# Kernel tuning notes

Hardware: AMD Instinct MI355X
Metric: run time of the kernel (lower is better)

The kernel has to match this reference:

```python
import jax, jax.numpy as jnp
import numpy as np

B, T, D = 4, 4000, 1024
H = 8
DK = D // H          # key dim per head; value dim per head also DK (value_factor=1)
CHUNK = 500
EPS_LN = 1e-5
EPS_RMS = 1e-6


def rotate_every_two(x):
    x1 = x[..., ::2]
    x2 = x[..., 1::2]
    return jnp.stack((-x2, x1), axis=-1).reshape(x.shape)


def theta_shift(x, sin, cos):
    # x: [b,h,t,dk]; sin/cos: [t,dk]
    return x * cos + rotate_every_two(x) * sin


def rel_pos(slen, chunk_len, num_heads, key_dim):
    # RetNetRelPos(chunkwise_recurrent=True)
    angle = 1.0 / (10000 ** jnp.linspace(0.0, 1.0, key_dim // 2))
    angle = jnp.repeat(angle, 2)  # == unsqueeze(-1).repeat(1,2).flatten()
    decay = jnp.log(1.0 - 2.0 ** (-5.0 - jnp.arange(num_heads, dtype=jnp.float32)))
    index = jnp.arange(slen, dtype=jnp.float32)
    sin = jnp.sin(index[:, None] * angle[None, :])  # [t,dk]
    cos = jnp.cos(index[:, None] * angle[None, :])
    bi = jnp.arange(chunk_len, dtype=jnp.float32)
    tril = jnp.tril(jnp.ones((chunk_len, chunk_len), bool))
    diff = bi[:, None] - bi[None, :]
    mask = jnp.where(tril[None], jnp.exp(decay[:, None, None] * diff[None]), 0.0)  # [H,C,C]
    last_row = mask[:, -1]                                            # [H,C]
    value_inner_decay = (last_row / last_row.sum(-1, keepdims=True))[:, :, None]  # [H,C,1]
    scale = jnp.sqrt(mask.sum(-1, keepdims=True))                     # [H,C,1]
    inner_mask = mask / scale
    cross_decay = jnp.exp(decay * chunk_len)[:, None, None]           # [H,1,1]
    qid = jnp.exp(decay[:, None] * (bi + 1.0))[:, :, None]            # [H,C,1]
    query_inner_decay = qid / (scale / last_row.sum(-1)[:, None, None])
    return (sin, cos), (inner_mask, cross_decay, query_inner_decay, value_inner_decay)


def retention_chunkwise(qr, kr, v, inner):
    mask, cross_decay, query_inner_decay, value_inner_decay = inner
    b, t = v.shape[0], v.shape[1]
    C = mask.shape[1]
    n = t // C
    h, dk = qr.shape[1], qr.shape[3]
    dv = v.shape[2] // h
    # [b,h,t,dk] -> [b,n,h,C,dk]
    qr = qr.transpose(0, 2, 1, 3).reshape(b, n, C, h, dk).transpose(0, 1, 3, 2, 4)
    kr = kr.transpose(0, 2, 1, 3).reshape(b, n, C, h, dk).transpose(0, 1, 3, 2, 4)
    v = v.reshape(b, n, C, h, dv).transpose(0, 1, 3, 2, 4)  # [b,n,h,C,dv]

    qk = jnp.einsum('bnhcd,bnhed->bnhce', qr, kr) * mask  # [b,n,h,C,C]
    inner_scale = jnp.clip(jnp.abs(jax.lax.stop_gradient(qk)).sum(-1, keepdims=True), 1.0, None)
    qk = qk / inner_scale
    inner_output = jnp.einsum('bnhce,bnhed->bnhcd', qk, v)  # [b,n,h,C,dv]

    kv = jnp.einsum('bnhck,bnhcv->bnhkv', kr, v * value_inner_decay)  # [b,n,h,dk,dv]

    def step(carry, kv_i):
        kv_state, kv_scale = carry
        out = (kv_state / kv_scale, kv_scale)
        new_state = kv_state * cross_decay + kv_i
        sg = jnp.abs(jax.lax.stop_gradient(new_state)).sum(-2, keepdims=True).max(-1, keepdims=True)
        return (new_state, jnp.clip(sg, 1.0, None)), out

    init = (jnp.zeros((b, h, dk, dv), v.dtype), jnp.ones((b, h, 1, 1), v.dtype))
    _, (kv_rec, cross_scale) = jax.lax.scan(step, init, jnp.moveaxis(kv, 1, 0))
    kv_rec = jnp.moveaxis(kv_rec, 0, 1)            # [b,n,h,dk,dv]
    cross_scale = jnp.moveaxis(cross_scale, 0, 1)  # [b,n,h,1,1]

    all_scale = jnp.maximum(inner_scale, cross_scale)
    cross_output = jnp.einsum('bnhcd,bnhdv->bnhcv', qr * query_inner_decay, kv_rec)
    output = inner_output / (all_scale / inner_scale) + cross_output / (all_scale / cross_scale)
    return output.transpose(0, 1, 3, 2, 4).reshape(b, t, h, dv)  # [b,t,h,dv]


def setup_inputs() -> dict:
    key = jax.random.key(0)
    ks = jax.random.split(key, 6)
    s = 0.02
    return {
        'inputs': jax.random.normal(ks[0], (B, T, D), jnp.float32),
        'ln_gamma': jnp.ones((D,), jnp.float32),
        'ln_beta': jnp.zeros((D,), jnp.float32),
        'Wq': jax.random.normal(ks[1], (D, D), jnp.float32) * s,
        'Wk': jax.random.normal(ks[2], (D, D), jnp.float32) * s,
        'Wv': jax.random.normal(ks[3], (D, D), jnp.float32) * s,
        'Wg': jax.random.normal(ks[4], (D, D), jnp.float32) * s,
        'Wo': jax.random.normal(ks[5], (D, D), jnp.float32) * s,
    }


def reference(inputs, ln_gamma, ln_beta, Wq, Wk, Wv, Wg, Wo):
    b, t, d = inputs.shape
    # pre-LayerNorm
    mu = inputs.mean(-1, keepdims=True)
    var = ((inputs - mu) ** 2).mean(-1, keepdims=True)
    x = (inputs - mu) / jnp.sqrt(var + EPS_LN) * ln_gamma + ln_beta

    (sin, cos), inner = rel_pos(t, CHUNK, H, DK)

    q = (x @ Wq).reshape(b, t, H, DK).transpose(0, 2, 1, 3)
    k = (x @ Wk * (DK ** -0.5)).reshape(b, t, H, DK).transpose(0, 2, 1, 3)
    v = x @ Wv
    g = x @ Wg

    qr = theta_shift(q, sin, cos)
    kr = theta_shift(k, sin, cos)

    out = retention_chunkwise(qr, kr, v, inner)  # [b,t,H,dv]
    # group norm: per-head RMSNorm without affine
    out = out * jax.lax.rsqrt(jnp.mean(out ** 2, -1, keepdims=True) + EPS_RMS)
    out = out.reshape(b, t, H * DK)
    out = jax.nn.silu(g) * out
    return out @ Wo  # dropout is identity in eval
```

## Files before the change

### kernel.cpp

```cpp
#include <hip/hip_runtime.h>
#include <hip/hip_bf16.h>


typedef __attribute__((ext_vector_type(4))) float f32x4;
typedef __attribute__((ext_vector_type(8))) short s16x8;

#define DEV static __device__ __forceinline__

DEV float bfu(ushort u){ union{uint i; float f;} x; x.i=((uint)u)<<16; return x.f; }
DEV ushort f2bf(float f){ union{float f; uint u;} x; x.f=f; uint r = x.u + 0x7fffu + ((x.u>>16)&1u); return (ushort)(r>>16); }
DEV uint pack2(float lo, float hi){ return ((uint)f2bf(hi)<<16) | (uint)f2bf(lo); }

DEV void gload16(const ushort* g, ushort* l) {
  __builtin_amdgcn_global_load_lds((const __attribute__((address_space(1))) void*)g,
                                   (__attribute__((address_space(3))) void*)l, 16, 0, 0);
}

__global__ __launch_bounds__(256) void f2bf_t_all(const float* __restrict__ s0, const float* __restrict__ s1,
                                                  const float* __restrict__ s2, const float* __restrict__ s3,
                                                  const float* __restrict__ s4,
                                                  ushort* __restrict__ d0, ushort* __restrict__ d1,
                                                  ushort* __restrict__ d2, ushort* __restrict__ d3,
                                                  ushort* __restrict__ d4) {
  const float* src; ushort* dst;
  switch (blockIdx.z) {
    case 0: src=s0; dst=d0; break;
    case 1: src=s1; dst=d1; break;
    case 2: src=s2; dst=d2; break;
    case 3: src=s3; dst=d3; break;
    default: src=s4; dst=d4; break;
  }
  __shared__ ushort t[64][72];
  int kt = blockIdx.x*64, nt = blockIdx.y*64;
  int tid = threadIdx.x;
  int r = tid>>2, c0 = (tid&3)*16;
  const float* s = src + (size_t)(kt+r)*1024 + nt + c0;
  #pragma unroll
  for (int j=0;j<16;j+=4) {
    float4 vv = *(const float4*)(s+j);
    t[r][c0+j]=f2bf(vv.x); t[r][c0+j+1]=f2bf(vv.y); t[r][c0+j+2]=f2bf(vv.z); t[r][c0+j+3]=f2bf(vv.w);
  }
  __syncthreads();
  union { uint4 u4[2]; ushort s16[16]; } tmp;
  #pragma unroll
  for (int j=0;j<16;j++) tmp.s16[j] = t[c0+j][r];
  ushort* d = dst + (size_t)(nt+r)*1024 + kt + c0;
  *(uint4*)(d)   = tmp.u4[0];
  *(uint4*)(d+8) = tmp.u4[1];
}

__global__ __launch_bounds__(256) void ln_kernel(const float* __restrict__ x,
                                                 const float* __restrict__ gamma,
                                                 const float* __restrict__ beta,
                                                 ushort* __restrict__ xo) {
  int row = blockIdx.x;
  int tid = threadIdx.x;
  const float* xr = x + (size_t)row*1024;
  float4 u = ((const float4*)xr)[tid];
  float s = u.x+u.y+u.z+u.w;
  float sq = u.x*u.x+u.y*u.y+u.z*u.z+u.w*u.w;
  #pragma unroll
  for (int o=32;o;o>>=1){ s += __shfl_xor(s,o); sq += __shfl_xor(sq,o); }
  __shared__ float red[8];
  int wv=tid>>6, ln=tid&63;
  if (ln==0){ red[wv]=s; red[4+wv]=sq; }
  __syncthreads();
  s = red[0]+red[1]+red[2]+red[3];
  sq = red[4]+red[5]+red[6]+red[7];
  float mu = s*(1.0f/1024.0f);
  float var = sq*(1.0f/1024.0f)-mu*mu;
  float inv = rsqrtf(var+1e-5f);
  float4 gg = ((const float4*)gamma)[tid];
  float4 bb = ((const float4*)beta)[tid];
  float o0=(u.x-mu)*inv*gg.x+bb.x;
  float o1=(u.y-mu)*inv*gg.y+bb.y;
  float o2=(u.z-mu)*inv*gg.z+bb.z;
  float o3=(u.w-mu)*inv*gg.w+bb.w;
  uint2 w; w.x=pack2(o0,o1); w.y=pack2(o2,o3);
  ((uint2*)(xo+(size_t)row*1024))[tid]=w;
}

__global__ __launch_bounds__(256) void sincos_kernel(float* __restrict__ sint, float* __restrict__ cost) {
  int idx = blockIdx.x*256+threadIdx.x;
  if (idx >= 4000*64) return;
  int t = idx>>6, i = idx&63;
  float ang = expf(-9.210340371976184f * (float)i * (1.0f/63.0f));
  float a = (float)t * ang;
  float sv = sinf(a), cv = cosf(a);
  sint[(size_t)t*128+2*i] = sv; sint[(size_t)t*128+2*i+1] = sv;
  cost[(size_t)t*128+2*i] = cv; cost[(size_t)t*128+2*i+1] = cv;
}

template<int EPI>
__global__ __launch_bounds__(256) void gemm_bt(const ushort* __restrict__ A,
                                               const ushort* __restrict__ BT,
                                               void* __restrict__ Cv,
                                               ushort* __restrict__ kTout,
                                               const float* __restrict__ sint,
                                               const float* __restrict__ cost,
                                               int M, int N, int K) {
  __shared__ ushort As[8192];
  __shared__ ushort Bs[8192];
  int ny = N>>7;
  int cpx = ((M>>7)*ny)>>3;
  int wg = blockIdx.x;
  int orig = (wg&7)*cpx + (wg>>3);
  int bm = (orig>>3)*128, bn = (orig&7)*128;
  int tid = threadIdx.x;
  int w = tid>>6, l = tid&63;
  int wm = (w>>1)*64, wn = (w&1)*64;
  int rsel = l&15, ko = (l>>4)*8;
  f32x4 acc[4][4];
  #pragma unroll
  for (int i=0;i<4;i++)
    #pragma unroll
    for (int j=0;j<4;j++){ acc[i][j][0]=0; acc[i][j][1]=0; acc[i][j][2]=0; acc[i][j][3]=0; }
  const ushort* ap0 = A  + (size_t)(bm + w*32 + (l>>2))*K + (l&3)*8;
  const ushort* ap1 = ap0 + (size_t)16*K;
  const ushort* bp0 = BT + (size_t)(bn + w*32 + (l>>2))*K + (l&3)*8;
  const ushort* bp1 = bp0 + (size_t)16*K;
  {
    ushort* ab = As + w*1024; ushort* bb = Bs + w*1024;
    gload16(ap0, ab); gload16(ap1, ab+512);
    gload16(bp0, bb); gload16(bp1, bb+512);
  }
  int cur = 0;
  for (int kt=0; kt<K; kt+=32) {
    __syncthreads();
    if (kt+32 < K) {
      int nb = cur^1;
      ushort* ab = As + nb*4096 + w*1024; ushort* bb = Bs + nb*4096 + w*1024;
      gload16(ap0+kt+32, ab); gload16(ap1+kt+32, ab+512);
      gload16(bp0+kt+32, bb); gload16(bp1+kt+32, bb+512);
    }
    const ushort* Ac = As + cur*4096;
    const ushort* Bc = Bs + cur*4096;
    s16x8 af[4], bfr[4];
    #pragma unroll
    for (int mf=0;mf<4;mf++) af[mf]  = *(const s16x8*)&Ac[(wm+mf*16+rsel)*32 + ko];
    #pragma unroll
    for (int nf=0;nf<4;nf++) bfr[nf] = *(const s16x8*)&Bc[(wn+nf*16+rsel)*32 + ko];
    #pragma unroll
    for (int mf=0;mf<4;mf++)
      #pragma unroll
      for (int nf=0;nf<4;nf++)
        acc[mf][nf] = __builtin_amdgcn_mfma_f32_16x16x32_bf16(af[mf], bfr[nf], acc[mf][nf], 0,0,0);
    cur ^= 1;
  }
  int crow0 = bm+wm+(l>>4)*4;
  int ccol0 = bn+wn+(l&15);
  #pragma unroll
  for (int mf=0;mf<4;mf++) {
    #pragma unroll
    for (int nf=0;nf<4;nf++) {
      int col = ccol0 + nf*16;
      if constexpr (EPI==0) {
        ushort* C = (ushort*)Cv;
        #pragma unroll
        for (int r2=0;r2<4;r2++)
          C[(size_t)(crow0+mf*16+r2)*N + col] = f2bf(acc[mf][nf][r2]);
      } else if constexpr (EPI==1) {
        float* C = (float*)Cv;
        #pragma unroll
        for (int r2=0;r2<4;r2++)
          C[(size_t)(crow0+mf*16+r2)*N + col] = acc[mf][nf][r2];
      } else if constexpr (EPI==2 || EPI==3) {
        ushort* C = (ushort*)Cv;
        int h = col>>7, d = col&127;
        float decay = logf(1.0f - exp2f(-5.0f-(float)h));
        #pragma unroll
        for (int r2=0;r2<4;r2++) {
          int row = crow0+mf*16+r2;
          int t = row - (row/4000)*4000;
          float cc = cost[(size_t)t*128+d], ss = sint[(size_t)t*128+d];
          float vv = acc[mf][nf][r2];
          float ov = __shfl_xor(vv, 1);
          float rot = ((l&1)==0) ? (vv*cc - ov*ss) : (vv*cc + ov*ss);
          int cch = t - (t/500)*500;
          if constexpr (EPI==2) {
            rot *= expf(decay*(float)cch);
            C[(size_t)row*N + col] = f2bf(rot);
          } else {
            rot *= expf(-decay*(float)cch) * 0.08838834764831845f;
            ushort rb = f2bf(rot);
            C[(size_t)row*N + col] = rb;
            int bnh = (row/4000)*64 + (t/500)*8 + h;
            kTout[(size_t)bnh*65536 + (size_t)d*512 + cch] = rb;
          }
        }
      } else {
        ushort* vTo = (ushort*)Cv;
        int h = col>>7, d = col&127;
        #pragma unroll
        for (int r2=0;r2<4;r2++) {
          int row = crow0+mf*16+r2;
          int t = row - (row/4000)*4000;
          int bnh = (row/4000)*64 + (t/500)*8 + h;
          int cch = t - (t/500)*500;
          vTo[(size_t)bnh*65536 + (size_t)d*512 + cch] = f2bf(acc[mf][nf][r2]);
        }
      }
    }
  }
}

__global__ __launch_bounds__(256) void kv_mfma(const ushort* __restrict__ kT,
                                               const ushort* __restrict__ vT,
                                               float* __restrict__ kvp) {
  int bnh = blockIdx.x;
  __shared__ ushort sh2[16384];
  int tid=threadIdx.x;
  int wv=tid>>6, l=tid&63, g=l>>4, c16=l&15;
  int wr = wv>>1, wc = wv&1;
  int ri[4], ro[4];
  #pragma unroll
  for (int jj=0;jj<4;jj++){
    int i = wv*256 + jj*64 + l;
    ri[jj] = i>>3;
    ro[jj] = (((i&7)*16) ^ ((ri[jj]&7)<<4))>>1;
  }
  const ushort* kbase = kT + (size_t)bnh*65536;
  const ushort* vbase = vT + (size_t)bnh*65536;
  f32x4 acc[4][4];
  #pragma unroll
  for (int i=0;i<4;i++)
    #pragma unroll
    for (int j=0;j<4;j++){ acc[i][j][0]=0; acc[i][j][1]=0; acc[i][j][2]=0; acc[i][j][3]=0; }
  for (int ctep=0; ctep<8; ctep++) {
    int cb = ctep*64;
    __syncthreads();
    #pragma unroll
    for (int jj=0;jj<4;jj++){
      gload16(kbase + (size_t)ri[jj]*512 + cb + ro[jj], (ushort*)((char*)sh2 + wv*4096 + jj*1024));
      gload16(vbase + (size_t)ri[jj]*512 + cb + ro[jj], (ushort*)((char*)sh2 + 16384 + wv*4096 + jj*1024));
    }
    __syncthreads();
    if (ctep==7) {
      for (int z=tid; z<128*12; z+=256) {
        int r = z/12, j = 52 + (z - (z/12)*12);
        *(ushort*)((char*)sh2 + 16384 + r*128 + ((j*2) ^ ((r&7)<<4))) = 0;
      }
      __syncthreads();
    }
    #pragma unroll
    for (int kc=0;kc<2;kc++) {
      s16x8 af[4], bf2[4];
      #pragma unroll
      for (int mf=0;mf<4;mf++){
        int row = wr*64+mf*16+c16;
        af[mf] = *(const s16x8*)((const char*)sh2 + row*128 + ((((kc*32+g*8)*2)) ^ ((row&7)<<4)));
      }
      #pragma unroll
      for (int nf=0;nf<4;nf++){
        int row = wc*64+nf*16+c16;
        bf2[nf] = *(const s16x8*)((const char*)sh2 + 16384 + row*128 + ((((kc*32+g*8)*2)) ^ ((row&7)<<4)));
      }
      #pragma unroll
      for (int mf=0;mf<4;mf++)
        #pragma unroll
        for (int nf=0;nf<4;nf++)
          acc[mf][nf] = __builtin_amdgcn_mfma_f32_16x16x32_bf16(af[mf], bf2[nf], acc[mf][nf], 0,0,0);
    }
  }
  float* outp = kvp + (size_t)bnh*16384;
  #pragma unroll
  for (int mf=0;mf<4;mf++)
    #pragma unroll
    for (int nf=0;nf<4;nf++)
      #pragma unroll
      for (int reg=0;reg<4;reg++)
        outp[(size_t)(wr*64+mf*16+g*4+reg)*128 + wc*64+nf*16+c16] = acc[mf][nf][reg];
}

__global__ __launch_bounds__(256) void scan_kernel(const float* __restrict__ kvp,
                                                   ushort* __restrict__ kvrecT,
                                                   float* __restrict__ crosssc) {
  int bh = blockIdx.x;
  int b = bh>>3, h = bh&7;
  float Dh = 1.0f - exp2f(-5.0f-(float)h);
  float decay = logf(Dh);
  float cd = expf(decay*500.0f);
  float ls = (1.0f - expf(decay*500.0f))/(1.0f-Dh);
  float cst = expf(decay*499.0f)/ls;
  int tid=threadIdx.x;
  int vcol = tid&127, khalf = tid>>7;
  float st[64];
  #pragma unroll
  for (int i=0;i<64;i++) st[i]=0;
  float scale = 1.0f;
  __shared__ float colpart[2][128];
  __shared__ float sred[2];
  for (int n=0;n<8;n++) {
    int bnh = (b*8+n)*8+h;
    const float* src = kvp + (size_t)bnh*16384;
    ushort* rec = kvrecT + (size_t)bnh*16384;
    float inv = 1.0f/scale;
    float cs = 0;
    #pragma unroll
    for (int i=0;i<64;i++) {
      int kk = khalf*64+i;
      rec[(size_t)vcol*128+kk] = f2bf(st[i]*inv);
      st[i] = st[i]*cd + cst*src[(size_t)kk*128+vcol];
      cs += fabsf(st[i]);
    }
    if (tid==0) crosssc[bnh] = scale;
    colpart[khalf][vcol] = cs;
    __syncthreads();
    if (tid<128) colpart[0][tid] += colpart[1][tid];
    __syncthreads();
    float m = (tid<128)? colpart[0][tid] : 0.0f;
    #pragma unroll
    for (int o=32;o;o>>=1) m = fmaxf(m,__shfl_xor(m,o));
    if (tid<128 && (tid&63)==0) sred[tid>>6]=m;
    __syncthreads();
    scale = fmaxf(fmaxf(sred[0],sred[1]),1.0f);
    __syncthreads();
  }
}

__global__ __launch_bounds__(256,4) void iout_mfma(const ushort* __restrict__ qr,
                                                   const ushort* __restrict__ kr,
                                                   const ushort* __restrict__ vT,
                                                   const ushort* __restrict__ kvrecT,
                                                   const float* __restrict__ crosssc,
                                                   const ushort* __restrict__ gbuf,
                                                   ushort* __restrict__ opre) {
  int ib = blockIdx.x;
  int x = ib&7, u = ib>>3;
  int rt = u&7;
  int bnh = x*32 + (u>>3);
  int h = bnh&7, n=(bnh>>3)&7, b=bnh>>6;
  size_t base = (size_t)(b*4000+n*500)*1024 + h*128;
  float Dh = 1.0f - exp2f(-5.0f-(float)h);
  float decay = logf(Dh);
  __shared__ ushort sh[20480];
  char* shb = (char*)sh;
  int tid = threadIdx.x;
  int wv = tid>>6, l = tid&63;
  int g = l>>4, c16 = l&15;
  int r_base = rt*64 + wv*16 + g*4;

  int qrow = rt*64 + wv*16 + c16; if (qrow>499) qrow=499;
  s16x8 aq[4];
  #pragma unroll
  for (int kc=0;kc<4;kc++)
    aq[kc] = *(const s16x8*)(qr + base + (size_t)qrow*1024 + kc*32 + g*8);

  int ktrow[4], ktofs[4], vtrow[4], vtofs[4];
  #pragma unroll
  for (int jj=0;jj<4;jj++){
    int i = wv*256 + jj*64 + l;
    int r_ = i>>4;  ktrow[jj]=r_;  ktofs[jj] = (((i&15)*16) ^ ((r_&7)<<4))>>1;
    int r2_ = i>>3; vtrow[jj]=r2_; vtofs[jj] = (((i&7)*16) ^ ((r2_&7)<<4))>>1;
  }
  const ushort* vTb = vT + (size_t)bnh*65536;

  f32x4 pv[8], cc[8];
  #pragma unroll
  for (int i=0;i<8;i++){
    #pragma unroll
    for (int j=0;j<4;j++){ pv[i][j]=0.0f; cc[i][j]=0.0f; }
  }
  float rowsum[4] = {0,0,0,0};

  for (int et=0; et<=rt; et++) {
    __syncthreads();
    #pragma unroll
    for (int jj=0;jj<4;jj++){
      int gr = et*64 + ktrow[jj]; if (gr>499) gr=499;
      gload16(kr + base + (size_t)gr*1024 + ktofs[jj], (ushort*)(shb + wv*4096 + jj*1024));
      gload16(vTb + (size_t)vtrow[jj]*512 + et*64 + vtofs[jj], (ushort*)(shb + 16384 + wv*4096 + jj*1024));
    }
    __syncthreads();
    f32x4 S[4];
    #pragma unroll
    for (int i=0;i<4;i++){ S[i][0]=0; S[i][1]=0; S[i][2]=0; S[i][3]=0; }
    __builtin_amdgcn_s_setprio(1);
    #pragma unroll
    for (int kc=0;kc<4;kc++) {
      #pragma unroll
      for (int ni=0;ni<4;ni++) {
        int krow = ni*16+c16;
        s16x8 bf = *(const s16x8*)(shb + krow*256 + ((((kc*32+g*8)*2)) ^ ((krow&7)<<4)));
        S[ni] = __builtin_amdgcn_mfma_f32_16x16x32_bf16(aq[kc], bf, S[ni], 0,0,0);
      }
    }
    __builtin_amdgcn_s_setprio(0);
    bool diag = (et==rt);
    #pragma unroll
    for (int ni=0;ni<4;ni++) {
      int e_rel = et*64 + ni*16 + c16;
      #pragma unroll
      for (int reg=0;reg<4;reg++) {
        float p = S[ni][reg];
        if (diag && e_rel > r_base+reg) p = 0.0f;
        rowsum[reg] += fabsf(p);
        int prow = wv*16 + g*4 + reg;
        *(ushort*)(shb + 32768 + prow*128 + (((ni*16+c16)*2) ^ ((prow&7)<<4))) = f2bf(p);
      }
    }
    __builtin_amdgcn_s_setprio(1);
    #pragma unroll
    for (int kc=0;kc<2;kc++) {
      int prow = wv*16 + c16;
      s16x8 pa = *(const s16x8*)(shb + 32768 + prow*128 + ((((kc*32+g*8)*2)) ^ ((prow&7)<<4)));
      #pragma unroll
      for (int nf=0;nf<8;nf++) {
        int vrow = nf*16+c16;
        s16x8 vb = *(const s16x8*)(shb + 16384 + vrow*128 + ((((kc*32+g*8)*2)) ^ ((vrow&7)<<4)));
        pv[nf] = __builtin_amdgcn_mfma_f32_16x16x32_bf16(pa, vb, pv[nf], 0,0,0);
      }
    }
    __builtin_amdgcn_s_setprio(0);
  }
  #pragma unroll
  for (int reg=0;reg<4;reg++) {
    float s = rowsum[reg];
    s += __shfl_xor(s,1); s += __shfl_xor(s,2); s += __shfl_xor(s,4); s += __shfl_xor(s,8);
    rowsum[reg] = s;
  }
  __syncthreads();
  #pragma unroll
  for (int jj=0;jj<8;jj++){
    int i = wv*512 + jj*64 + l;
    int r_ = i>>4;
    int ofs = (((i&15)*16) ^ ((r_&7)<<4))>>1;
    gload16(kvrecT + (size_t)bnh*16384 + (size_t)r_*128 + ofs, (ushort*)(shb + wv*8192 + jj*1024));
  }
  __syncthreads();
  __builtin_amdgcn_s_setprio(1);
  #pragma unroll
  for (int kc=0;kc<4;kc++) {
    #pragma unroll
    for (int nf=0;nf<8;nf++) {
      int krow = nf*16+c16;
      s16x8 bb = *(const s16x8*)(shb + krow*256 + ((((kc*32+g*8)*2)) ^ ((krow&7)<<4)));
      cc[nf] = __builtin_amdgcn_mfma_f32_16x16x32_bf16(aq[kc], bb, cc[nf], 0,0,0);
    }
  }
  __builtin_amdgcn_s_setprio(0);
  float cs = crosssc[bnh];
  float lsum = (1.0f-expf(decay*500.0f))/(1.0f-Dh);
  float ed = expf(decay);
  #pragma unroll
  for (int reg=0;reg<4;reg++) {
    int rr = r_base + reg;
    if (rr < 500) {
      float rs = (1.0f-expf(decay*(float)(rr+1)))/(1.0f-Dh);
      float rsr = rsqrtf(rs);
      float is = fmaxf(1.0f, rowsum[reg]*rsr);
      float all = fmaxf(is, cs);
      float qid = ed*lsum*rsr;
      float fi = rsr/all;
      float fc = qid*(cs/all);
      float o[8]; float ssq = 0.0f;
      #pragma unroll
      for (int nf=0;nf<8;nf++){ o[nf] = pv[nf][reg]*fi + cc[nf][reg]*fc; ssq += o[nf]*o[nf]; }
      ssq += __shfl_xor(ssq,1); ssq += __shfl_xor(ssq,2); ssq += __shfl_xor(ssq,4); ssq += __shfl_xor(ssq,8);
      float rmss = rsqrtf(ssq*(1.0f/128.0f)+1e-6f);
      size_t rowoff = (size_t)(b*4000+n*500+rr)*1024 + h*128;
      #pragma unroll
      for (int nf=0;nf<8;nf++){
        float gv = bfu(gbuf[rowoff + nf*16 + c16]);
        float sg = gv/(1.0f+expf(-gv));
        opre[rowoff + nf*16 + c16] = f2bf(sg*o[nf]*rmss);
      }
    }
  }
}

extern "C" void kernel_launch(void* const* d_in, const int* in_sizes, int n_in,
                              void* d_out, int out_size, void* d_ws, size_t ws_size,
                              hipStream_t stream) {
  const float* x     = (const float*)d_in[0];
  const float* gamma = (const float*)d_in[1];
  const float* beta  = (const float*)d_in[2];
  const float* Wq    = (const float*)d_in[3];
  const float* Wk    = (const float*)d_in[4];
  const float* Wv    = (const float*)d_in[5];
  const float* Wg    = (const float*)d_in[6];
  const float* Wo    = (const float*)d_in[7];
  float* out = (float*)d_out;

  char* ws = (char*)d_ws;
  size_t off = 0;
  auto alloc = [&](size_t bytes)->void* { void* p = ws+off; off += (bytes+255)&~(size_t)255; return p; };
  const size_t BT1024 = (size_t)16000*1024;
  ushort* xln  = (ushort*)alloc(BT1024*2);
  ushort* q    = (ushort*)alloc(BT1024*2);
  ushort* k    = (ushort*)alloc(BT1024*2);
  ushort* g    = (ushort*)alloc(BT1024*2);
  ushort* WqT  = (ushort*)alloc((size_t)1024*1024*2);
  ushort* WkT  = (ushort*)alloc((size_t)1024*1024*2);
  ushort* WvT  = (ushort*)alloc((size_t)1024*1024*2);
  ushort* WgT  = (ushort*)alloc((size_t)1024*1024*2);
  ushort* WoT  = (ushort*)alloc((size_t)1024*1024*2);
  float* sint  = (float*)alloc((size_t)4000*128*4);
  float* cost  = (float*)alloc((size_t)4000*128*4);
  ushort* kT   = (ushort*)alloc((size_t)256*65536*2);
  ushort* vT   = (ushort*)alloc((size_t)256*65536*2);
  ushort* kvrecT=(ushort*)alloc((size_t)256*16384*2);
  float* crosssc = (float*)alloc(256*4);
  (void)ws_size; (void)in_sizes; (void)n_in; (void)out_size;

  ln_kernel<<<16000,256,0,stream>>>(x,gamma,beta,xln);
  sincos_kernel<<<1000,256,0,stream>>>(sint,cost);
  dim3 tt(16,16,5);
  f2bf_t_all<<<tt,256,0,stream>>>(Wq,Wk,Wv,Wg,Wo, WqT,WkT,WvT,WgT,WoT);

  gemm_bt<2><<<1000,256,0,stream>>>(xln,WqT,(void*)q, nullptr,sint,cost,16000,1024,1024);
  gemm_bt<3><<<1000,256,0,stream>>>(xln,WkT,(void*)k, kT,     sint,cost,16000,1024,1024);
  gemm_bt<4><<<1000,256,0,stream>>>(xln,WvT,(void*)vT,nullptr,sint,cost,16000,1024,1024);
  gemm_bt<0><<<1000,256,0,stream>>>(xln,WgT,(void*)g, nullptr,sint,cost,16000,1024,1024);

  float* kvp = (float*)xln;
  kv_mfma<<<256,256,0,stream>>>(kT,vT,kvp);
  scan_kernel<<<32,256,0,stream>>>(kvp,kvrecT,crosssc);

  ushort* opre = xln;
  iout_mfma<<<2048,256,0,stream>>>(q,k,vT,kvrecT,crosssc,g,opre);

  gemm_bt<1><<<1000,256,0,stream>>>(opre,WoT,(void*)out,nullptr,sint,cost,16000,1024,1024);
}
```

Baseline: 453.2 us.

## Fuse Q/K/V/G projections into one GEMM with LDS-staged coalesced epilogues

Replaces the four separate projection GEMM launches with one launch that treats the four transposed weight matrices as a single N=4096 operand. Each tile's output is staged through shared memory so q/k/g rows are written with 16-byte vector stores and the transposed kT/vT chunk layouts are written as packed 8-element vectors. Previously these were scattered 2-byte stores. The output GEMM also stages fp32 results through LDS for coalesced float4 writes. The fused kernel assumes WqT, WkT, WvT and WgT sit contiguously in the workspace, and it adds extra LDS use and barriers in the epilogue.

```diff
diff --git a/kernel.cpp b/kernel.cpp
--- a/kernel.cpp
+++ b/kernel.cpp
@@ -91,20 +91,145 @@
   cost[(size_t)t*128+2*i] = cv; cost[(size_t)t*128+2*i+1] = cv;
 }
 
-template<int EPI>
-__global__ __launch_bounds__(256) void gemm_bt(const ushort* __restrict__ A,
-                                               const ushort* __restrict__ BT,
-                                               void* __restrict__ Cv,
-                                               ushort* __restrict__ kTout,
-                                               const float* __restrict__ sint,
-                                               const float* __restrict__ cost,
-                                               int M, int N, int K) {
-  __shared__ ushort As[8192];
-  __shared__ ushort Bs[8192];
-  int ny = N>>7;
-  int cpx = ((M>>7)*ny)>>3;
+__global__ __launch_bounds__(256) void gemm_proj(const ushort* __restrict__ A,
+                                                 const ushort* __restrict__ BT,
+                                                 ushort* __restrict__ qb,
+                                                 ushort* __restrict__ kb,
+                                                 ushort* __restrict__ gb,
+                                                 ushort* __restrict__ kT,
+                                                 ushort* __restrict__ vT,
+                                                 const float* __restrict__ sint,
+                                                 const float* __restrict__ cost) {
+  __attribute__((aligned(16))) __shared__ char smem[34816];
+  ushort* As = (ushort*)smem;
+  ushort* Bs = (ushort*)(smem+16384);
+  const int K = 1024;
   int wg = blockIdx.x;
-  int orig = (wg&7)*cpx + (wg>>3);
+  int orig = (wg&7)*500 + (wg>>3);
+  int bm = (orig>>5)*128, bn = (orig&31)*128;
+  int tid = threadIdx.x;
+  int w = tid>>6, l = tid&63;
+  int wm = (w>>1)*64, wn = (w&1)*64;
+  int rsel = l&15, ko = (l>>4)*8;
+  f32x4 acc[4][4];
+  #pragma unroll
+  for (int i=0;i<4;i++)
+    #pragma unroll
+    for (int j=0;j<4;j++){ acc[i][j][0]=0; acc[i][j][1]=0; acc[i][j][2]=0; acc[i][j][3]=0; }
+  const ushort* ap0 = A  + (size_t)(bm + w*32 + (l>>2))*K + (l&3)*8;
+  const ushort* ap1 = ap0 + (size_t)16*K;
+  const ushort* bp0 = BT + (size_t)(bn + w*32 + (l>>2))*K + (l&3)*8;
+  const ushort* bp1 = bp0 + (size_t)16*K;
+  {
+    ushort* ab = As + w*1024; ushort* bb2 = Bs + w*1024;
+    gload16(ap0, ab); gload16(ap1, ab+512);
+    gload16(bp0, bb2); gload16(bp1, bb2+512);
+  }
+  int cur = 0;
+  for (int kt=0; kt<K; kt+=32) {
+    __syncthreads();
+    if (kt+32 < K) {
+      int nb = cur^1;
+      ushort* ab = As + nb*4096 + w*1024; ushort* bb2 = Bs + nb*4096 + w*1024;
+      gload16(ap0+kt+32, ab); gload16(ap1+kt+32, ab+512);
+      gload16(bp0+kt+32, bb2); gload16(bp1+kt+32, bb2+512);
+    }
+    const ushort* Ac = As + cur*4096;
+    const ushort* Bc = Bs + cur*4096;
+    s16x8 af[4], bfr[4];
+    #pragma unroll
+    for (int mf=0;mf<4;mf++) af[mf]  = *(const s16x8*)&Ac[(wm+mf*16+rsel)*32 + ko];
+    #pragma unroll
+    for (int nf=0;nf<4;nf++) bfr[nf] = *(const s16x8*)&Bc[(wn+nf*16+rsel)*32 + ko];
+    #pragma unroll
+    for (int mf=0;mf<4;mf++)
+      #pragma unroll
+      for (int nf=0;nf<4;nf++)
+        acc[mf][nf] = __builtin_amdgcn_mfma_f32_16x16x32_bf16(af[mf], bfr[nf], acc[mf][nf], 0,0,0);
+    cur ^= 1;
+  }
+  int proj = bn>>10;
+  int bnp  = bn&1023;
+  int hh   = bnp>>7;
+  __syncthreads();
+  ushort* Ct = (ushort*)smem;
+  if (proj < 2) {
+    float decay = logf(1.0f - exp2f(-5.0f-(float)hh));
+    float ksc = 0.08838834764831845f;
+    #pragma unroll
+    for (int mf=0;mf<4;mf++) {
+      #pragma unroll
+      for (int r2=0;r2<4;r2++) {
+        int rowt = wm+mf*16+(l>>4)*4+r2;
+        int grow = bm+rowt;
+        int t = grow - (grow/4000)*4000;
+        int cch = t - (t/500)*500;
+        float esc = (proj==0)? expf(decay*(float)cch) : expf(-decay*(float)cch)*ksc;
+        const float* ctab = cost + (size_t)t*128;
+        const float* stab = sint + (size_t)t*128;
+        #pragma unroll
+        for (int nf=0;nf<4;nf++) {
+          int colt = wn+nf*16+(l&15);
+          float vv = acc[mf][nf][r2];
+          float cc = ctab[colt], ss = stab[colt];
+          float ov = __shfl_xor(vv,1);
+          float rot = ((l&1)==0)? (vv*cc-ov*ss) : (vv*cc+ov*ss);
+          Ct[rowt*136+colt] = f2bf(rot*esc);
+        }
+      }
+    }
+  } else {
+    #pragma unroll
+    for (int mf=0;mf<4;mf++)
+      #pragma unroll
+      for (int nf=0;nf<4;nf++) {
+        int colt = wn+nf*16+(l&15);
+        #pragma unroll
+        for (int r2=0;r2<4;r2++)
+          Ct[(wm+mf*16+(l>>4)*4+r2)*136+colt] = f2bf(acc[mf][nf][r2]);
+      }
+  }
+  __syncthreads();
+  if (proj != 2) {
+    ushort* dst = (proj==0)? qb : (proj==1)? kb : gb;
+    int r = tid>>1, ch=(tid&1)*64;
+    ushort* drow = dst + (size_t)(bm+r)*1024 + bnp + ch;
+    #pragma unroll
+    for (int j=0;j<8;j++) *(uint4*)(drow+j*8) = *(uint4*)&Ct[r*136+ch+j*8];
+  }
+  if (proj==1 || proj==2) {
+    ushort* Tdst = (proj==1)? kT : vT;
+    int dloc = tid>>1, rh=(tid&1)*64;
+    #pragma unroll
+    for (int j=0;j<8;j++) {
+      int gr = bm + rh + j*8;
+      int bb = gr/4000; int t0 = gr - bb*4000;
+      int ch0 = t0/500; int c0 = t0 - ch0*500;
+      if (c0 <= 492) {
+        union{uint4 u; ushort s[8];} pk;
+        #pragma unroll
+        for (int i=0;i<8;i++) pk.s[i] = Ct[(rh+j*8+i)*136 + dloc];
+        *(uint4*)(Tdst + ((size_t)(bb*64+ch0*8+hh))*65536 + (size_t)dloc*512 + c0) = pk.u;
+      } else {
+        #pragma unroll
+        for (int i=0;i<8;i++) {
+          int gri = gr+i; int bbi=gri/4000; int ti=gri-bbi*4000; int chi=ti/500; int ci=ti-chi*500;
+          Tdst[((size_t)(bbi*64+chi*8+hh))*65536 + (size_t)dloc*512 + ci] = Ct[(rh+j*8+i)*136+dloc];
+        }
+      }
+    }
+  }
+}
+
+__global__ __launch_bounds__(256) void gemm_out(const ushort* __restrict__ A,
+                                                const ushort* __restrict__ BT,
+                                                float* __restrict__ C) {
+  __attribute__((aligned(16))) __shared__ char smem[34816];
+  ushort* As = (ushort*)smem;
+  ushort* Bs = (ushort*)(smem+16384);
+  const int K = 1024;
+  int wg = blockIdx.x;
+  int orig = (wg&7)*125 + (wg>>3);
   int bm = (orig>>3)*128, bn = (orig&7)*128;
   int tid = threadIdx.x;
   int w = tid>>6, l = tid&63;
@@ -120,18 +245,18 @@
   const ushort* bp0 = BT + (size_t)(bn + w*32 + (l>>2))*K + (l&3)*8;
   const ushort* bp1 = bp0 + (size_t)16*K;
   {
-    ushort* ab = As + w*1024; ushort* bb = Bs + w*1024;
+    ushort* ab = As + w*1024; ushort* bb2 = Bs + w*1024;
     gload16(ap0, ab); gload16(ap1, ab+512);
-    gload16(bp0, bb); gload16(bp1, bb+512);
+    gload16(bp0, bb2); gload16(bp1, bb2+512);
   }
   int cur = 0;
   for (int kt=0; kt<K; kt+=32) {
     __syncthreads();
     if (kt+32 < K) {
       int nb = cur^1;
-      ushort* ab = As + nb*4096 + w*1024; ushort* bb = Bs + nb*4096 + w*1024;
+      ushort* ab = As + nb*4096 + w*1024; ushort* bb2 = Bs + nb*4096 + w*1024;
       gload16(ap0+kt+32, ab); gload16(ap1+kt+32, ab+512);
-      gload16(bp0+kt+32, bb); gload16(bp1+kt+32, bb+512);
+      gload16(bp0+kt+32, bb2); gload16(bp1+kt+32, bb2+512);
     }
     const ushort* Ac = As + cur*4096;
     const ushort* Bc = Bs + cur*4096;
@@ -147,60 +272,27 @@
         acc[mf][nf] = __builtin_amdgcn_mfma_f32_16x16x32_bf16(af[mf], bfr[nf], acc[mf][nf], 0,0,0);
     cur ^= 1;
   }
-  int crow0 = bm+wm+(l>>4)*4;
-  int ccol0 = bn+wn+(l&15);
-  #pragma unroll
-  for (int mf=0;mf<4;mf++) {
-    #pragma unroll
-    for (int nf=0;nf<4;nf++) {
-      int col = ccol0 + nf*16;
-      if constexpr (EPI==0) {
-        ushort* C = (ushort*)Cv;
+  __syncthreads();
+  float* Cf = (float*)smem;
+  #pragma unroll
+  for (int half=0; half<2; half++) {
+    if ((w>>1)==half) {
+      #pragma unroll
+      for (int mf=0;mf<4;mf++)
         #pragma unroll
-        for (int r2=0;r2<4;r2++)
-          C[(size_t)(crow0+mf*16+r2)*N + col] = f2bf(acc[mf][nf][r2]);
-      } else if constexpr (EPI==1) {
-        float* C = (float*)Cv;
-        #pragma unroll
-        for (int r2=0;r2<4;r2++)
-          C[(size_t)(crow0+mf*16+r2)*N + col] = acc[mf][nf][r2];
-      } else if constexpr (EPI==2 || EPI==3) {
-        ushort* C = (ushort*)Cv;
-        int h = col>>7, d = col&127;
-        float decay = logf(1.0f - exp2f(-5.0f-(float)h));
-        #pragma unroll
-        for (int r2=0;r2<4;r2++) {
-          int row = crow0+mf*16+r2;
-          int t = row - (row/4000)*4000;
-          float cc = cost[(size_t)t*128+d], ss = sint[(size_t)t*128+d];
-          float vv = acc[mf][nf][r2];
-          float ov = __shfl_xor(vv, 1);
-          float rot = ((l&1)==0) ? (vv*cc - ov*ss) : (vv*cc + ov*ss);
-          int cch = t - (t/500)*500;
-          if constexpr (EPI==2) {
-            rot *= expf(decay*(float)cch);
-            C[(size_t)row*N + col] = f2bf(rot);
-          } else {
-            rot *= expf(-decay*(float)cch) * 0.08838834764831845f;
-            ushort rb = f2bf(rot);
-            C[(size_t)row*N + col] = rb;
-            int bnh = (row/4000)*64 + (t/500)*8 + h;
-            kTout[(size_t)bnh*65536 + (size_t)d*512 + cch] = rb;
-          }
-        }
-      } else {
-        ushort* vTo = (ushort*)Cv;
-        int h = col>>7, d = col&127;
-        #pragma unroll
-        for (int r2=0;r2<4;r2++) {
-          int row = crow0+mf*16+r2;
-          int t = row - (row/4000)*4000;
-          int bnh = (row/4000)*64 + (t/500)*8 + h;
-          int cch = t - (t/500)*500;
-          vTo[(size_t)bnh*65536 + (size_t)d*512 + cch] = f2bf(acc[mf][nf][r2]);
-        }
-      }
-    }
+        for (int nf=0;nf<4;nf++)
+          #pragma unroll
+          for (int r2=0;r2<4;r2++)
+            Cf[(mf*16+(l>>4)*4+r2)*132 + wn+nf*16+(l&15)] = acc[mf][nf][r2];
+    }
+    __syncthreads();
+    {
+      int r = tid>>2, cs=(tid&3)*32;
+      float* drow = C + (size_t)(bm+half*64+r)*1024 + bn + cs;
+      #pragma unroll
+      for (int j=0;j<8;j++) *(float4*)(drow+j*4) = *(float4*)&Cf[r*132+cs+j*4];
+    }
+    __syncthreads();
   }
 }
 
@@ -508,10 +600,7 @@
   dim3 tt(16,16,5);
   f2bf_t_all<<<tt,256,0,stream>>>(Wq,Wk,Wv,Wg,Wo, WqT,WkT,WvT,WgT,WoT);
 
-  gemm_bt<2><<<1000,256,0,stream>>>(xln,WqT,(void*)q, nullptr,sint,cost,16000,1024,1024);
-  gemm_bt<3><<<1000,256,0,stream>>>(xln,WkT,(void*)k, kT,     sint,cost,16000,1024,1024);
-  gemm_bt<4><<<1000,256,0,stream>>>(xln,WvT,(void*)vT,nullptr,sint,cost,16000,1024,1024);
-  gemm_bt<0><<<1000,256,0,stream>>>(xln,WgT,(void*)g, nullptr,sint,cost,16000,1024,1024);
+  gemm_proj<<<4000,256,0,stream>>>(xln, WqT, q, k, g, kT, vT, sint, cost);
 
   float* kvp = (float*)xln;
   kv_mfma<<<256,256,0,stream>>>(kT,vT,kvp);
@@ -520,5 +609,5 @@
   ushort* opre = xln;
   iout_mfma<<<2048,256,0,stream>>>(q,k,vT,kvrecT,crosssc,g,opre);
 
-  gemm_bt<1><<<1000,256,0,stream>>>(opre,WoT,(void*)out,nullptr,sint,cost,16000,1024,1024);
-}
+  gemm_out<<<1000,256,0,stream>>>(opre,WoT,out);
+}
```

Result: faster. 405.7 us (-10.5%).
